# Kernel tuning notes

Measured on AMD Instinct MI355X. Metric: run time of the kernel, lower is better.

The kernel has to match this reference:

```python
import jax, jax.numpy as jnp
import numpy as np

D = 1024
H = 16
MODES = 16
EPS = 1e-5


def _layernorm(x, g, b):
    mu = jnp.mean(x, axis=-1, keepdims=True)
    var = jnp.var(x, axis=-1, keepdims=True)
    return (x - mu) * jax.lax.rsqrt(var + EPS) * g + b


def setup_inputs() -> dict:
    key = jax.random.key(0)
    ks = jax.random.split(key, 12)
    B, S = 32, 2048
    x_feat = jax.random.normal(ks[0], (B, S, D), dtype=jnp.float32)
    z_prev = jax.random.normal(ks[1], (B, D), dtype=jnp.float32)
    # MultiheadAttention params (torch packs q,k,v in in_proj)
    in_proj_w = jax.random.normal(ks[2], (3 * D, D), dtype=jnp.float32) * (1.0 / np.sqrt(D))
    in_proj_b = jnp.zeros((3 * D,), dtype=jnp.float32)
    out_proj_w = jax.random.normal(ks[3], (D, D), dtype=jnp.float32) * (1.0 / np.sqrt(D))
    out_proj_b = jnp.zeros((D,), dtype=jnp.float32)
    ln1_g = jnp.ones((D,), jnp.float32); ln1_b = jnp.zeros((D,), jnp.float32)
    ln2_g = jnp.ones((D,), jnp.float32); ln2_b = jnp.zeros((D,), jnp.float32)
    scale_real = jax.random.normal(ks[4], (MODES, D), dtype=jnp.float32) * 0.02
    scale_imag = jax.random.normal(ks[5], (MODES, D), dtype=jnp.float32) * 0.02
    # spectral_norm(Linear): effective weight = W / sigma_max(W); bake it in
    Wp = np.asarray(jax.random.normal(ks[6], (D, D), dtype=jnp.float32)) * (1.0 / np.sqrt(D))
    sigma = np.linalg.svd(Wp, compute_uv=False)[0]
    proj_w = jnp.asarray(Wp / sigma, dtype=jnp.float32)
    proj_b = jnp.zeros((D,), jnp.float32)
    bn_g = jnp.ones((D,), jnp.float32); bn_b = jnp.zeros((D,), jnp.float32)
    gate = jnp.asarray(0.5, jnp.float32)
    scale_attn = jnp.ones((1,), jnp.float32)
    scale_denoise = jnp.ones((1,), jnp.float32)
    return dict(x_feat=x_feat, z_prev=z_prev, in_proj_w=in_proj_w, in_proj_b=in_proj_b,
                out_proj_w=out_proj_w, out_proj_b=out_proj_b, ln1_g=ln1_g, ln1_b=ln1_b,
                ln2_g=ln2_g, ln2_b=ln2_b, scale_real=scale_real, scale_imag=scale_imag,
                proj_w=proj_w, proj_b=proj_b, bn_g=bn_g, bn_b=bn_b, gate=gate,
                scale_attn=scale_attn, scale_denoise=scale_denoise)


def reference(x_feat, z_prev, in_proj_w, in_proj_b, out_proj_w, out_proj_b,
              ln1_g, ln1_b, ln2_g, ln2_b, scale_real, scale_imag,
              proj_w, proj_b, bn_g, bn_b, gate, scale_attn, scale_denoise):
    B, S, _ = x_feat.shape
    hd = D // H
    Wq, Wk, Wv = in_proj_w[:D], in_proj_w[D:2 * D], in_proj_w[2 * D:]
    bq, bk, bv = in_proj_b[:D], in_proj_b[D:2 * D], in_proj_b[2 * D:]
    # single-query cross attention: q from z_prev [B,D], k/v from x_feat [B,S,D]
    q = (z_prev @ Wq.T + bq).reshape(B, H, hd)
    k = (x_feat @ Wk.T + bk).reshape(B, S, H, hd)
    v = (x_feat @ Wv.T + bv).reshape(B, S, H, hd)
    scores = jnp.einsum('bhd,bshd->bhs', q, k) / np.sqrt(hd)
    attn = jax.nn.softmax(scores, axis=-1)
    ctx = jnp.einsum('bhs,bshd->bhd', attn, v).reshape(B, D)
    attn_out = ctx @ out_proj_w.T + out_proj_b
    z1 = _layernorm(z_prev + scale_attn * attn_out, ln1_g, ln1_b)  # [B,D]
    # fft_denoise: keep first MODES freqs, each scaled by mean of its complex filter row
    filt = jnp.mean(scale_real + 1j * scale_imag, axis=1)  # [MODES] complex
    fvec = jnp.zeros((D,), dtype=jnp.complex64).at[:MODES].set(filt.astype(jnp.complex64))
    z_freq = jnp.fft.fft(z1, axis=1) * fvec[None, :]
    z_spatial = jnp.fft.ifft(z_freq, axis=1).real.astype(z1.dtype)
    denoised = z_spatial @ proj_w.T + proj_b
    z2 = _layernorm(z1 + scale_denoise * denoised, ln2_g, ln2_b)
    g = jax.nn.sigmoid(gate)
    z3 = g * z2 + (1.0 - g) * z_prev
    # BatchNorm1d (training-mode batch stats, biased variance)
    mu = jnp.mean(z3, axis=0, keepdims=True)
    var = jnp.var(z3, axis=0, keepdims=True)
    out = (z3 - mu) * jax.lax.rsqrt(var + EPS) * bn_g + bn_b
    return out
```

## Files before the change

### kernel.cpp

```cpp
#include <hip/hip_runtime.h>

#define B_ 32
#define S_ 2048
#define D_ 1024
#define H_ 16
#define HD_ 64
#define MODES_ 16
#define EPS_ 1e-5f

#define NSPLIT_ 16
#define RPB_ 128
#define RPI_ 32
#define NIT_ (RPB_ / RPI_)

#define OFF_CK      32
#define OFF_Q       1024
#define OFF_QKBF    33792
#define OFF_ML      295936
#define ML_L_OFF    8192
#define OFF_PART_F  312320
#define OFF_CTX     4506624
#define OFF_R1      4539392
#define OFF_Z1      4572160
#define OFF_ZSP     4604928
#define OFF_R2      4637696
#define OFF_Z3      4670464

typedef __attribute__((ext_vector_type(8))) short short8v;
typedef __attribute__((ext_vector_type(4))) float f32x4;

static __device__ inline unsigned short f2bf(float f) {
    union { float f; unsigned u; } v; v.f = f;
    unsigned r = v.u + 0x7FFFu + ((v.u >> 16) & 1u);
    return (unsigned short)(r >> 16);
}
static __device__ inline float bf2f(unsigned s) {
    union { unsigned u; float f; } v; v.u = s << 16;
    return v.f;
}

__global__ void k_q(const float* __restrict__ zprev, const float* __restrict__ ipw,
                    const float* __restrict__ ipb, float* __restrict__ q_out,
                    float* __restrict__ ck_out) {
    int b = blockIdx.x >> 2, nc = blockIdx.x & 3;
    __shared__ float zr[D_];
    int t = threadIdx.x;
    for (int i = t; i < D_; i += 256) zr[i] = zprev[(size_t)b * D_ + i];
    __syncthreads();
    int n = nc * 256 + t;
    const float4* wr = (const float4*)(ipw + (size_t)n * D_);
    float acc = 0.f;
    for (int k = 0; k < D_ / 4; ++k) {
        float4 wv = wr[k];
        float4 zv = *(const float4*)&zr[4 * k];
        acc = fmaf(zv.x, wv.x, acc); acc = fmaf(zv.y, wv.y, acc);
        acc = fmaf(zv.z, wv.z, acc); acc = fmaf(zv.w, wv.w, acc);
    }
    float qv = acc + ipb[n];
    q_out[(size_t)b * D_ + n] = qv;
    float cv = qv * ipb[D_ + n];
#pragma unroll
    for (int o = 32; o > 0; o >>= 1) cv += __shfl_xor(cv, o);
    if ((t & 63) == 0) ck_out[b * H_ + (n >> 6)] = cv;
}

__global__ void k_qkc(const float* __restrict__ ipw, const float* __restrict__ q_in,
                      unsigned short* __restrict__ qk_out) {
    int bid = blockIdx.x;
    int bc = bid & 3, nc = (bid >> 2) & 3, h = bid >> 4;
    int t = threadIdx.x;
    __shared__ float4 tile4[HD_ * 64];
    __shared__ float qall[8 * HD_];
    const float4* wk4 = (const float4*)(ipw + (size_t)D_ * D_);
#pragma unroll
    for (int j = 0; j < 16; ++j) {
        int lin4 = j * 256 + t;
        int i = lin4 >> 6, n4 = lin4 & 63;
        tile4[lin4] = wk4[(size_t)(h * HD_ + i) * 256 + nc * 64 + n4];
    }
#pragma unroll
    for (int j = 0; j < 2; ++j) {
        int idx = j * 256 + t;
        int bb = idx >> 6, i = idx & 63;
        qall[idx] = q_in[(size_t)(bc * 8 + bb) * D_ + h * HD_ + i];
    }
    __syncthreads();
    const float* tile = (const float*)tile4;
#pragma unroll
    for (int bb = 0; bb < 8; ++bb) {
        float acc = 0.f;
#pragma unroll
        for (int i = 0; i < HD_; ++i) acc = fmaf(qall[bb * HD_ + i], tile[i * 256 + t], acc);
        int b = bc * 8 + bb;
        qk_out[(size_t)(b * H_ + h) * D_ + nc * 256 + t] = f2bf(acc);
    }
}

__global__ __launch_bounds__(256, 2) void k_attn(const float* __restrict__ xfeat,
        const unsigned short* __restrict__ qkbf, const float* __restrict__ ck,
        unsigned short* __restrict__ part, float* __restrict__ ml) {
    int bid = blockIdx.x;
    int c = bid & (NSPLIT_ - 1), b = bid >> 4;
    int t = threadIdx.x, w = t >> 6, l = t & 63;
    __shared__ unsigned char xbuf[RPI_ * 2048];
    __shared__ float Sred[4][RPI_][16];
    __shared__ unsigned short Pt[16][RPI_];
    __shared__ float mh[16], lh[16], fh[16], ckl[16];

    if (t < 16) { mh[t] = -1e30f; lh[t] = 0.f; ckl[t] = ck[b * H_ + t]; }

    f32x4 acc[16];
#pragma unroll
    for (int nt = 0; nt < 16; ++nt) acc[nt] = (f32x4){0.f, 0.f, 0.f, 0.f};

    int hr = l & 15, kg = l >> 4;
    const unsigned short* qkb = qkbf + ((size_t)(b * H_ + hr) << 10);

    for (int it = 0; it < NIT_; ++it) {
        __syncthreads();
        {
            const float4* src = (const float4*)(xfeat + ((size_t)b * S_ + c * RPB_ + it * RPI_) * D_);
#pragma unroll 4
            for (int j = 0; j < 32; ++j) {
                int idx = j * 256 + t;
                float4 v = src[idx];
                int row = idx >> 8, dq = idx & 255;
                unsigned off = (unsigned)(row * 2048 + dq * 8) ^ (unsigned)((row & 7) << 4);
                ushort4 u;
                u.x = f2bf(v.x); u.y = f2bf(v.y); u.z = f2bf(v.z); u.w = f2bf(v.w);
                *(ushort4*)(xbuf + off) = u;
            }
        }
        __syncthreads();
        {
            f32x4 s0 = {0.f, 0.f, 0.f, 0.f}, s1 = {0.f, 0.f, 0.f, 0.f};
#pragma unroll
            for (int ks = 0; ks < 8; ++ks) {
                int k = w * 256 + ks * 32 + kg * 8;
                short8v bq = *(const short8v*)(qkb + k);
                unsigned off0 = (unsigned)(hr * 2048 + k * 2) ^ (unsigned)((hr & 7) << 4);
                short8v a0 = *(const short8v*)(xbuf + off0);
                short8v a1 = *(const short8v*)(xbuf + (off0 ^ 32768u));
                s0 = __builtin_amdgcn_mfma_f32_16x16x32_bf16(a0, bq, s0, 0, 0, 0);
                s1 = __builtin_amdgcn_mfma_f32_16x16x32_bf16(a1, bq, s1, 0, 0, 0);
            }
            int rbase = kg * 4;
#pragma unroll
            for (int r = 0; r < 4; ++r) {
                Sred[w][rbase + r][hr] = s0[r];
                Sred[w][16 + rbase + r][hr] = s1[r];
            }
        }
        __syncthreads();
        {
            int h = t >> 4, i16 = t & 15;
            float sv0 = Sred[0][i16][h] + Sred[1][i16][h] + Sred[2][i16][h] + Sred[3][i16][h];
            float sv1 = Sred[0][i16 + 16][h] + Sred[1][i16 + 16][h] + Sred[2][i16 + 16][h] + Sred[3][i16 + 16][h];
            float s0 = (sv0 + ckl[h]) * 0.125f;
            float s1 = (sv1 + ckl[h]) * 0.125f;
            float mm = fmaxf(s0, s1);
#pragma unroll
            for (int o = 8; o > 0; o >>= 1) mm = fmaxf(mm, __shfl_xor(mm, o, 16));
            float mold = mh[h];
            float mnew = fmaxf(mold, mm);
            float p0 = __expf(s0 - mnew), p1 = __expf(s1 - mnew);
            Pt[h][i16] = f2bf(p0); Pt[h][i16 + 16] = f2bf(p1);
            float ps = p0 + p1;
#pragma unroll
            for (int o = 8; o > 0; o >>= 1) ps += __shfl_xor(ps, o, 16);
            if (i16 == 0) {
                float f = __expf(mold - mnew);
                fh[h] = f; lh[h] = lh[h] * f + ps; mh[h] = mnew;
            }
        }
        __syncthreads();
        {
            float f0 = fh[kg * 4 + 0], f1 = fh[kg * 4 + 1], f2 = fh[kg * 4 + 2], f3 = fh[kg * 4 + 3];
#pragma unroll
            for (int nt = 0; nt < 16; ++nt) {
                acc[nt][0] *= f0; acc[nt][1] *= f1; acc[nt][2] *= f2; acc[nt][3] *= f3;
            }
            short8v pa = *(const short8v*)(&Pt[hr][kg * 8]);
#pragma unroll
            for (int nt = 0; nt < 16; ++nt) {
                int d = w * 256 + nt * 16 + hr;
                unsigned short xb[8];
#pragma unroll
                for (int j = 0; j < 8; ++j) {
                    int s = kg * 8 + j;
                    unsigned off = (unsigned)(s * 2048 + d * 2) ^ (unsigned)((s & 7) << 4);
                    xb[j] = *(const unsigned short*)(xbuf + off);
                }
                short8v bx;
                bx[0] = (short)xb[0]; bx[1] = (short)xb[1]; bx[2] = (short)xb[2]; bx[3] = (short)xb[3];
                bx[4] = (short)xb[4]; bx[5] = (short)xb[5]; bx[6] = (short)xb[6]; bx[7] = (short)xb[7];
                acc[nt] = __builtin_amdgcn_mfma_f32_16x16x32_bf16(pa, bx, acc[nt], 0, 0, 0);
            }
        }
    }
    {
#pragma unroll
        for (int nt = 0; nt < 16; ++nt) {
            int d = w * 256 + nt * 16 + hr;
#pragma unroll
            for (int r = 0; r < 4; ++r) {
                int h = kg * 4 + r;
                part[(((size_t)(c * B_ + b) * H_ + h) << 10) + d] = f2bf(acc[nt][r]);
            }
        }
        if (t < 16) {
            ml[(size_t)(c * B_ + b) * H_ + t] = mh[t];
            ml[ML_L_OFF + (size_t)(c * B_ + b) * H_ + t] = lh[t];
        }
    }
}

__global__ void k_ctx2(const float* __restrict__ ipw, const float* __restrict__ ipb,
                       const unsigned short* __restrict__ part, const float* __restrict__ ml,
                       float* __restrict__ ctx) {
    int b = blockIdx.x >> 2, nc = blockIdx.x & 3;
    int t = threadIdx.x;
    __shared__ float mls[4][16], lls[4][16], coef[4][16];
    __shared__ float xr[4 * D_];
    if (t < 64) {
        int h4 = t >> 4, c = t & 15;
        mls[h4][c] = ml[(size_t)(c * B_ + b) * H_ + nc * 4 + h4];
        lls[h4][c] = ml[ML_L_OFF + (size_t)(c * B_ + b) * H_ + nc * 4 + h4];
    }
    __syncthreads();
    if (t < 4) {
        float M = -1e30f;
        for (int c = 0; c < 16; ++c) M = fmaxf(M, mls[t][c]);
        float L = 0.f;
        for (int c = 0; c < 16; ++c) L += lls[t][c] * __expf(mls[t][c] - M);
        float invL = 1.f / L;
        for (int c = 0; c < 16; ++c) coef[t][c] = __expf(mls[t][c] - M) * invL;
    }
    __syncthreads();
    for (int idx = t * 2; idx < 4 * D_; idx += 512) {
        int h4 = idx >> 10, d = idx & 1023;
        int h = nc * 4 + h4;
        float a0 = 0.f, a1 = 0.f;
        for (int c = 0; c < 16; ++c) {
            unsigned u = *(const unsigned*)&part[(((size_t)(c * B_ + b) * H_ + h) << 10) + d];
            float cf = coef[h4][c];
            a0 = fmaf(bf2f(u & 0xffffu), cf, a0);
            a1 = fmaf(bf2f(u >> 16), cf, a1);
        }
        xr[idx] = a0; xr[idx + 1] = a1;
    }
    __syncthreads();
    int n = nc * 256 + t;
    int hl = t >> 6;
    const float4* wr = (const float4*)(ipw + ((size_t)2 * D_ + n) * D_);
    const float4* xv4 = (const float4*)&xr[hl * D_];
    float acc = 0.f;
    for (int k = 0; k < D_ / 4; ++k) {
        float4 wv = wr[k], xv = xv4[k];
        acc = fmaf(wv.x, xv.x, acc); acc = fmaf(wv.y, xv.y, acc);
        acc = fmaf(wv.z, xv.z, acc); acc = fmaf(wv.w, xv.w, acc);
    }
    ctx[(size_t)b * D_ + n] = acc + ipb[2 * D_ + n];
}

__global__ void k_proj_res(const float* __restrict__ wmat, const float* __restrict__ bias,
                           const float* __restrict__ scale, const float* __restrict__ resid,
                           const float* __restrict__ invec, float* __restrict__ outvec) {
    int b = blockIdx.x >> 2, nc = blockIdx.x & 3;
    __shared__ float cx[D_];
    int t = threadIdx.x;
    for (int i = t; i < D_; i += 256) cx[i] = invec[(size_t)b * D_ + i];
    __syncthreads();
    int n = nc * 256 + t;
    const float4* wr = (const float4*)(wmat + (size_t)n * D_);
    float acc = 0.f;
    for (int k = 0; k < D_ / 4; ++k) {
        float4 wv = wr[k];
        float4 cv = *(const float4*)&cx[4 * k];
        acc = fmaf(wv.x, cv.x, acc); acc = fmaf(wv.y, cv.y, acc);
        acc = fmaf(wv.z, cv.z, acc); acc = fmaf(wv.w, cv.w, acc);
    }
    outvec[(size_t)b * D_ + n] = resid[(size_t)b * D_ + n] + scale[0] * (acc + bias[n]);
}

__global__ void k_ln(const float* __restrict__ inv, const float* __restrict__ g,
                     const float* __restrict__ bv, float* __restrict__ outv) {
    int b = blockIdx.x, t = threadIdx.x, w = t >> 6, l = t & 63;
    float4 v = ((const float4*)(inv + (size_t)b * D_))[t];
    float s = v.x + v.y + v.z + v.w;
    float s2 = v.x * v.x + v.y * v.y + v.z * v.z + v.w * v.w;
    __shared__ float sa[4], sb[4];
#pragma unroll
    for (int o = 32; o > 0; o >>= 1) { s += __shfl_xor(s, o); s2 += __shfl_xor(s2, o); }
    if (l == 0) { sa[w] = s; sb[w] = s2; }
    __syncthreads();
    s = sa[0] + sa[1] + sa[2] + sa[3];
    s2 = sb[0] + sb[1] + sb[2] + sb[3];
    float mu = s * (1.f / (float)D_);
    float var = s2 * (1.f / (float)D_) - mu * mu;
    float rs = rsqrtf(var + EPS_);
    float4 gg = ((const float4*)g)[t], bb = ((const float4*)bv)[t];
    float4 o4;
    o4.x = (v.x - mu) * rs * gg.x + bb.x;
    o4.y = (v.y - mu) * rs * gg.y + bb.y;
    o4.z = (v.z - mu) * rs * gg.z + bb.z;
    o4.w = (v.w - mu) * rs * gg.w + bb.w;
    ((float4*)(outv + (size_t)b * D_))[t] = o4;
}

__global__ void k_spec(const float* __restrict__ sreal, const float* __restrict__ simag,
                       float* __restrict__ ws) {
    int b = blockIdx.x, t = threadIdx.x;
    __shared__ float zr[D_];
    __shared__ float fre[MODES_], fim[MODES_];
    __shared__ float cre[MODES_], cim[MODES_];
    const float* z1 = ws + OFF_Z1 + (size_t)b * D_;
    for (int i = t; i < D_; i += 256) zr[i] = z1[i];
    int m = t >> 4, sub = t & 15;
    {
        float ar = 0.f, ai = 0.f;
        for (int k = sub; k < D_; k += 16) { ar += sreal[m * D_ + k]; ai += simag[m * D_ + k]; }
#pragma unroll
        for (int o = 8; o > 0; o >>= 1) { ar += __shfl_xor(ar, o, 16); ai += __shfl_xor(ai, o, 16); }
        if (sub == 0) { fre[m] = ar * (1.f / (float)D_); fim[m] = ai * (1.f / (float)D_); }
    }
    __syncthreads();
    const float step = 6.283185307179586f / (float)D_;
    float ar = 0.f, ai = 0.f;
    for (int n = sub; n < D_; n += 16) {
        int idx = (m * n) & (D_ - 1);
        float sn, cs;
        __sincosf(step * (float)idx, &sn, &cs);
        float z = zr[n];
        ar = fmaf(z, cs, ar); ai = fmaf(-z, sn, ai);
    }
#pragma unroll
    for (int o = 8; o > 0; o >>= 1) { ar += __shfl_xor(ar, o, 16); ai += __shfl_xor(ai, o, 16); }
    if (sub == 0) {
        cre[m] = (fre[m] * ar - fim[m] * ai) * (1.f / (float)D_);
        cim[m] = (fre[m] * ai + fim[m] * ar) * (1.f / (float)D_);
    }
    __syncthreads();
    for (int n = t; n < D_; n += 256) {
        float acc = 0.f;
#pragma unroll
        for (int mm = 0; mm < MODES_; ++mm) {
            int idx = (mm * n) & (D_ - 1);
            float sn, cs;
            __sincosf(step * (float)idx, &sn, &cs);
            acc += cre[mm] * cs - cim[mm] * sn;
        }
        ws[OFF_ZSP + (size_t)b * D_ + n] = acc;
    }
}

__global__ void k_ln2gate(const float* __restrict__ zprev, const float* __restrict__ g2,
                          const float* __restrict__ b2v, const float* __restrict__ gate,
                          float* __restrict__ ws) {
    int b = blockIdx.x, t = threadIdx.x, w = t >> 6, l = t & 63;
    float4 v = ((const float4*)(ws + OFF_R2 + (size_t)b * D_))[t];
    float s = v.x + v.y + v.z + v.w;
    float s2 = v.x * v.x + v.y * v.y + v.z * v.z + v.w * v.w;
    __shared__ float sa[4], sb[4];
#pragma unroll
    for (int o = 32; o > 0; o >>= 1) { s += __shfl_xor(s, o); s2 += __shfl_xor(s2, o); }
    if (l == 0) { sa[w] = s; sb[w] = s2; }
    __syncthreads();
    s = sa[0] + sa[1] + sa[2] + sa[3];
    s2 = sb[0] + sb[1] + sb[2] + sb[3];
    float mu = s * (1.f / (float)D_);
    float var = s2 * (1.f / (float)D_) - mu * mu;
    float rs = rsqrtf(var + EPS_);
    float4 gg = ((const float4*)g2)[t], bb = ((const float4*)b2v)[t];
    float gsig = 1.f / (1.f + __expf(-gate[0]));
    float4 zp = ((const float4*)(zprev + (size_t)b * D_))[t];
    float4 z3;
    z3.x = gsig * ((v.x - mu) * rs * gg.x + bb.x) + (1.f - gsig) * zp.x;
    z3.y = gsig * ((v.y - mu) * rs * gg.y + bb.y) + (1.f - gsig) * zp.y;
    z3.z = gsig * ((v.z - mu) * rs * gg.z + bb.z) + (1.f - gsig) * zp.z;
    z3.w = gsig * ((v.w - mu) * rs * gg.w + bb.w) + (1.f - gsig) * zp.w;
    ((float4*)(ws + OFF_Z3 + (size_t)b * D_))[t] = z3;
}

__global__ void k_bn(const float* __restrict__ bng, const float* __restrict__ bnb,
                     const float* __restrict__ z3, float* __restrict__ out) {
    int d = blockIdx.x * 256 + threadIdx.x;
    float vals[B_];
    float s = 0.f, s2 = 0.f;
#pragma unroll
    for (int b = 0; b < B_; ++b) {
        float v = z3[(size_t)b * D_ + d];
        vals[b] = v; s += v; s2 = fmaf(v, v, s2);
    }
    float mu = s * (1.f / (float)B_);
    float var = s2 * (1.f / (float)B_) - mu * mu;
    float rs = rsqrtf(var + EPS_);
    float gg = bng[d], bb = bnb[d];
#pragma unroll
    for (int b = 0; b < B_; ++b) out[(size_t)b * D_ + d] = (vals[b] - mu) * rs * gg + bb;
}

extern "C" void kernel_launch(void* const* d_in, const int* in_sizes, int n_in,
                              void* d_out, int out_size, void* d_ws, size_t ws_size,
                              hipStream_t stream) {
    const float* x_feat = (const float*)d_in[0];
    const float* z_prev = (const float*)d_in[1];
    const float* ipw    = (const float*)d_in[2];
    const float* ipb    = (const float*)d_in[3];
    const float* wout   = (const float*)d_in[4];
    const float* bout   = (const float*)d_in[5];
    const float* ln1g   = (const float*)d_in[6];
    const float* ln1b   = (const float*)d_in[7];
    const float* ln2g   = (const float*)d_in[8];
    const float* ln2b   = (const float*)d_in[9];
    const float* sreal  = (const float*)d_in[10];
    const float* simag  = (const float*)d_in[11];
    const float* pw     = (const float*)d_in[12];
    const float* pb     = (const float*)d_in[13];
    const float* bng    = (const float*)d_in[14];
    const float* bnb    = (const float*)d_in[15];
    const float* gate   = (const float*)d_in[16];
    const float* sattn  = (const float*)d_in[17];
    const float* sden   = (const float*)d_in[18];
    float* ws  = (float*)d_ws;
    float* out = (float*)d_out;
    unsigned short* qkbf  = (unsigned short*)(ws + OFF_QKBF);
    unsigned short* partp = (unsigned short*)(ws + OFF_PART_F);

    k_q<<<B_ * 4, 256, 0, stream>>>(z_prev, ipw, ipb, ws + OFF_Q, ws + OFF_CK);
    k_qkc<<<H_ * 16, 256, 0, stream>>>(ipw, ws + OFF_Q, qkbf);
    k_attn<<<B_ * NSPLIT_, 256, 0, stream>>>(x_feat, qkbf, ws + OFF_CK, partp, ws + OFF_ML);
    k_ctx2<<<B_ * 4, 256, 0, stream>>>(ipw, ipb, partp, ws + OFF_ML, ws + OFF_CTX);
    k_proj_res<<<B_ * 4, 256, 0, stream>>>(wout, bout, sattn, z_prev, ws + OFF_CTX, ws + OFF_R1);
    k_ln<<<B_, 256, 0, stream>>>(ws + OFF_R1, ln1g, ln1b, ws + OFF_Z1);
    k_spec<<<B_, 256, 0, stream>>>(sreal, simag, ws);
    k_proj_res<<<B_ * 4, 256, 0, stream>>>(pw, pb, sden, ws + OFF_Z1, ws + OFF_ZSP, ws + OFF_R2);
    k_ln2gate<<<B_, 256, 0, stream>>>(z_prev, ln2g, ln2b, gate, ws);
    k_bn<<<D_ / 256, 256, 0, stream>>>(bng, bnb, ws + OFF_Z3, out);
}
```

Before: 259.5 us.

## Fuse layernorm with spectral filter and add ILP, hoisted Q fragments, packed bf16 converts

```diff
diff --git a/kernel.cpp b/kernel.cpp
--- a/kernel.cpp
+++ b/kernel.cpp
@@ -1,4 +1,5 @@
 #include <hip/hip_runtime.h>
+#include <hip/hip_bf16.h>
 
 #define B_ 32
 #define S_ 2048
@@ -29,10 +30,13 @@
 typedef __attribute__((ext_vector_type(8))) short short8v;
 typedef __attribute__((ext_vector_type(4))) float f32x4;
 
-static __device__ inline unsigned short f2bf(float f) {
-    union { float f; unsigned u; } v; v.f = f;
-    unsigned r = v.u + 0x7FFFu + ((v.u >> 16) & 1u);
-    return (unsigned short)(r >> 16);
+static __device__ inline ushort2 f2bf2(float a, float b) {
+    __hip_bfloat162 h = __float22bfloat162_rn(make_float2(a, b));
+    union { __hip_bfloat162 h; ushort2 u; } v; v.h = h; return v.u;
+}
+static __device__ inline unsigned short f2bf(float a) {
+    __hip_bfloat16 h = __float2bfloat16(a);
+    union { __hip_bfloat16 h; unsigned short u; } v; v.h = h; return v.u;
 }
 static __device__ inline float bf2f(unsigned s) {
     union { unsigned u; float f; } v; v.u = s << 16;
@@ -49,14 +53,19 @@
     __syncthreads();
     int n = nc * 256 + t;
     const float4* wr = (const float4*)(ipw + (size_t)n * D_);
-    float acc = 0.f;
-    for (int k = 0; k < D_ / 4; ++k) {
-        float4 wv = wr[k];
-        float4 zv = *(const float4*)&zr[4 * k];
-        acc = fmaf(zv.x, wv.x, acc); acc = fmaf(zv.y, wv.y, acc);
-        acc = fmaf(zv.z, wv.z, acc); acc = fmaf(zv.w, wv.w, acc);
-    }
-    float qv = acc + ipb[n];
+    float a0 = 0.f, a1 = 0.f, a2 = 0.f, a3 = 0.f;
+    for (int k = 0; k < 256; k += 4) {
+        float4 w0 = wr[k], w1 = wr[k + 1], w2 = wr[k + 2], w3 = wr[k + 3];
+        float4 z0 = *(const float4*)&zr[4 * k];
+        float4 z1 = *(const float4*)&zr[4 * k + 4];
+        float4 z2 = *(const float4*)&zr[4 * k + 8];
+        float4 z3 = *(const float4*)&zr[4 * k + 12];
+        a0 = fmaf(z0.x, w0.x, a0); a0 = fmaf(z0.y, w0.y, a0); a0 = fmaf(z0.z, w0.z, a0); a0 = fmaf(z0.w, w0.w, a0);
+        a1 = fmaf(z1.x, w1.x, a1); a1 = fmaf(z1.y, w1.y, a1); a1 = fmaf(z1.z, w1.z, a1); a1 = fmaf(z1.w, w1.w, a1);
+        a2 = fmaf(z2.x, w2.x, a2); a2 = fmaf(z2.y, w2.y, a2); a2 = fmaf(z2.z, w2.z, a2); a2 = fmaf(z2.w, w2.w, a2);
+        a3 = fmaf(z3.x, w3.x, a3); a3 = fmaf(z3.y, w3.y, a3); a3 = fmaf(z3.z, w3.z, a3); a3 = fmaf(z3.w, w3.w, a3);
+    }
+    float qv = (a0 + a1) + (a2 + a3) + ipb[n];
     q_out[(size_t)b * D_ + n] = qv;
     float cv = qv * ipb[D_ + n];
 #pragma unroll
@@ -88,11 +97,14 @@
     const float* tile = (const float*)tile4;
 #pragma unroll
     for (int bb = 0; bb < 8; ++bb) {
-        float acc = 0.f;
-#pragma unroll
-        for (int i = 0; i < HD_; ++i) acc = fmaf(qall[bb * HD_ + i], tile[i * 256 + t], acc);
+        float a0 = 0.f, a1 = 0.f;
+#pragma unroll
+        for (int i = 0; i < HD_; i += 2) {
+            a0 = fmaf(qall[bb * HD_ + i], tile[i * 256 + t], a0);
+            a1 = fmaf(qall[bb * HD_ + i + 1], tile[(i + 1) * 256 + t], a1);
+        }
         int b = bc * 8 + bb;
-        qk_out[(size_t)(b * H_ + h) * D_ + nc * 256 + t] = f2bf(acc);
+        qk_out[(size_t)(b * H_ + h) * D_ + nc * 256 + t] = f2bf(a0 + a1);
     }
 }
 
@@ -103,7 +115,7 @@
     int c = bid & (NSPLIT_ - 1), b = bid >> 4;
     int t = threadIdx.x, w = t >> 6, l = t & 63;
     __shared__ unsigned char xbuf[RPI_ * 2048];
-    __shared__ float Sred[4][RPI_][16];
+    __shared__ float Sred[4][RPI_][17];
     __shared__ unsigned short Pt[16][RPI_];
     __shared__ float mh[16], lh[16], fh[16], ckl[16];
 
@@ -115,19 +127,23 @@
 
     int hr = l & 15, kg = l >> 4;
     const unsigned short* qkb = qkbf + ((size_t)(b * H_ + hr) << 10);
+    short8v qfrag[8];
+#pragma unroll
+    for (int ks = 0; ks < 8; ++ks)
+        qfrag[ks] = *(const short8v*)(qkb + w * 256 + ks * 32 + kg * 8);
 
     for (int it = 0; it < NIT_; ++it) {
         __syncthreads();
         {
             const float4* src = (const float4*)(xfeat + ((size_t)b * S_ + c * RPB_ + it * RPI_) * D_);
-#pragma unroll 4
+#pragma unroll 8
             for (int j = 0; j < 32; ++j) {
                 int idx = j * 256 + t;
                 float4 v = src[idx];
                 int row = idx >> 8, dq = idx & 255;
                 unsigned off = (unsigned)(row * 2048 + dq * 8) ^ (unsigned)((row & 7) << 4);
-                ushort4 u;
-                u.x = f2bf(v.x); u.y = f2bf(v.y); u.z = f2bf(v.z); u.w = f2bf(v.w);
+                ushort2 lo = f2bf2(v.x, v.y), hi = f2bf2(v.z, v.w);
+                ushort4 u; u.x = lo.x; u.y = lo.y; u.z = hi.x; u.w = hi.y;
                 *(ushort4*)(xbuf + off) = u;
             }
         }
@@ -137,12 +153,11 @@
 #pragma unroll
             for (int ks = 0; ks < 8; ++ks) {
                 int k = w * 256 + ks * 32 + kg * 8;
-                short8v bq = *(const short8v*)(qkb + k);
                 unsigned off0 = (unsigned)(hr * 2048 + k * 2) ^ (unsigned)((hr & 7) << 4);
                 short8v a0 = *(const short8v*)(xbuf + off0);
                 short8v a1 = *(const short8v*)(xbuf + (off0 ^ 32768u));
-                s0 = __builtin_amdgcn_mfma_f32_16x16x32_bf16(a0, bq, s0, 0, 0, 0);
-                s1 = __builtin_amdgcn_mfma_f32_16x16x32_bf16(a1, bq, s1, 0, 0, 0);
+                s0 = __builtin_amdgcn_mfma_f32_16x16x32_bf16(a0, qfrag[ks], s0, 0, 0, 0);
+                s1 = __builtin_amdgcn_mfma_f32_16x16x32_bf16(a1, qfrag[ks], s1, 0, 0, 0);
             }
             int rbase = kg * 4;
 #pragma unroll
@@ -184,16 +199,13 @@
 #pragma unroll
             for (int nt = 0; nt < 16; ++nt) {
                 int d = w * 256 + nt * 16 + hr;
-                unsigned short xb[8];
+                short8v bx;
 #pragma unroll
                 for (int j = 0; j < 8; ++j) {
                     int s = kg * 8 + j;
                     unsigned off = (unsigned)(s * 2048 + d * 2) ^ (unsigned)((s & 7) << 4);
-                    xb[j] = *(const unsigned short*)(xbuf + off);
+                    bx[j] = *(const short*)(xbuf + off);
                 }
-                short8v bx;
-                bx[0] = (short)xb[0]; bx[1] = (short)xb[1]; bx[2] = (short)xb[2]; bx[3] = (short)xb[3];
-                bx[4] = (short)xb[4]; bx[5] = (short)xb[5]; bx[6] = (short)xb[6]; bx[7] = (short)xb[7];
                 acc[nt] = __builtin_amdgcn_mfma_f32_16x16x32_bf16(pa, bx, acc[nt], 0, 0, 0);
             }
         }
@@ -254,13 +266,16 @@
     int hl = t >> 6;
     const float4* wr = (const float4*)(ipw + ((size_t)2 * D_ + n) * D_);
     const float4* xv4 = (const float4*)&xr[hl * D_];
-    float acc = 0.f;
-    for (int k = 0; k < D_ / 4; ++k) {
-        float4 wv = wr[k], xv = xv4[k];
-        acc = fmaf(wv.x, xv.x, acc); acc = fmaf(wv.y, xv.y, acc);
-        acc = fmaf(wv.z, xv.z, acc); acc = fmaf(wv.w, xv.w, acc);
-    }
-    ctx[(size_t)b * D_ + n] = acc + ipb[2 * D_ + n];
+    float a0 = 0.f, a1 = 0.f, a2 = 0.f, a3 = 0.f;
+    for (int k = 0; k < 256; k += 4) {
+        float4 w0 = wr[k], w1 = wr[k + 1], w2 = wr[k + 2], w3 = wr[k + 3];
+        float4 x0 = xv4[k], x1 = xv4[k + 1], x2 = xv4[k + 2], x3 = xv4[k + 3];
+        a0 = fmaf(w0.x, x0.x, a0); a0 = fmaf(w0.y, x0.y, a0); a0 = fmaf(w0.z, x0.z, a0); a0 = fmaf(w0.w, x0.w, a0);
+        a1 = fmaf(w1.x, x1.x, a1); a1 = fmaf(w1.y, x1.y, a1); a1 = fmaf(w1.z, x1.z, a1); a1 = fmaf(w1.w, x1.w, a1);
+        a2 = fmaf(w2.x, x2.x, a2); a2 = fmaf(w2.y, x2.y, a2); a2 = fmaf(w2.z, x2.z, a2); a2 = fmaf(w2.w, x2.w, a2);
+        a3 = fmaf(w3.x, x3.x, a3); a3 = fmaf(w3.y, x3.y, a3); a3 = fmaf(w3.z, x3.z, a3); a3 = fmaf(w3.w, x3.w, a3);
+    }
+    ctx[(size_t)b * D_ + n] = (a0 + a1) + (a2 + a3) + ipb[2 * D_ + n];
 }
 
 __global__ void k_proj_res(const float* __restrict__ wmat, const float* __restrict__ bias,
@@ -273,72 +288,76 @@
     __syncthreads();
     int n = nc * 256 + t;
     const float4* wr = (const float4*)(wmat + (size_t)n * D_);
-    float acc = 0.f;
-    for (int k = 0; k < D_ / 4; ++k) {
-        float4 wv = wr[k];
-        float4 cv = *(const float4*)&cx[4 * k];
-        acc = fmaf(wv.x, cv.x, acc); acc = fmaf(wv.y, cv.y, acc);
-        acc = fmaf(wv.z, cv.z, acc); acc = fmaf(wv.w, cv.w, acc);
-    }
+    float a0 = 0.f, a1 = 0.f, a2 = 0.f, a3 = 0.f;
+    for (int k = 0; k < 256; k += 4) {
+        float4 w0 = wr[k], w1 = wr[k + 1], w2 = wr[k + 2], w3 = wr[k + 3];
+        float4 c0 = *(const float4*)&cx[4 * k];
+        float4 c1 = *(const float4*)&cx[4 * k + 4];
+        float4 c2 = *(const float4*)&cx[4 * k + 8];
+        float4 c3 = *(const float4*)&cx[4 * k + 12];
+        a0 = fmaf(w0.x, c0.x, a0); a0 = fmaf(w0.y, c0.y, a0); a0 = fmaf(w0.z, c0.z, a0); a0 = fmaf(w0.w, c0.w, a0);
+        a1 = fmaf(w1.x, c1.x, a1); a1 = fmaf(w1.y, c1.y, a1); a1 = fmaf(w1.z, c1.z, a1); a1 = fmaf(w1.w, c1.w, a1);
+        a2 = fmaf(w2.x, c2.x, a2); a2 = fmaf(w2.y, c2.y, a2); a2 = fmaf(w2.z, c2.z, a2); a2 = fmaf(w2.w, c2.w, a2);
+        a3 = fmaf(w3.x, c3.x, a3); a3 = fmaf(w3.y, c3.y, a3); a3 = fmaf(w3.z, c3.z, a3); a3 = fmaf(w3.w, c3.w, a3);
+    }
+    float acc = (a0 + a1) + (a2 + a3);
     outvec[(size_t)b * D_ + n] = resid[(size_t)b * D_ + n] + scale[0] * (acc + bias[n]);
 }
 
-__global__ void k_ln(const float* __restrict__ inv, const float* __restrict__ g,
-                     const float* __restrict__ bv, float* __restrict__ outv) {
+__global__ void k_lnspec(const float* __restrict__ r1, const float* __restrict__ g1,
+                         const float* __restrict__ b1, const float* __restrict__ sreal,
+                         const float* __restrict__ simag, float* __restrict__ z1out,
+                         float* __restrict__ zspout) {
     int b = blockIdx.x, t = threadIdx.x, w = t >> 6, l = t & 63;
-    float4 v = ((const float4*)(inv + (size_t)b * D_))[t];
+    __shared__ float zr[D_];
+    __shared__ float fre[MODES_], fim[MODES_];
+    __shared__ float cre[MODES_], cim[MODES_];
+    __shared__ float sa[4], sb[4];
+    float4 v = ((const float4*)(r1 + (size_t)b * D_))[t];
     float s = v.x + v.y + v.z + v.w;
     float s2 = v.x * v.x + v.y * v.y + v.z * v.z + v.w * v.w;
-    __shared__ float sa[4], sb[4];
 #pragma unroll
     for (int o = 32; o > 0; o >>= 1) { s += __shfl_xor(s, o); s2 += __shfl_xor(s2, o); }
     if (l == 0) { sa[w] = s; sb[w] = s2; }
+    int m = t >> 4, sub = t & 15;
+    {
+        float ar = 0.f, ai = 0.f;
+        for (int k = sub; k < D_; k += 16) { ar += sreal[m * D_ + k]; ai += simag[m * D_ + k]; }
+#pragma unroll
+        for (int o = 8; o > 0; o >>= 1) { ar += __shfl_xor(ar, o, 16); ai += __shfl_xor(ai, o, 16); }
+        if (sub == 0) { fre[m] = ar * (1.f / (float)D_); fim[m] = ai * (1.f / (float)D_); }
+    }
     __syncthreads();
     s = sa[0] + sa[1] + sa[2] + sa[3];
     s2 = sb[0] + sb[1] + sb[2] + sb[3];
     float mu = s * (1.f / (float)D_);
     float var = s2 * (1.f / (float)D_) - mu * mu;
     float rs = rsqrtf(var + EPS_);
-    float4 gg = ((const float4*)g)[t], bb = ((const float4*)bv)[t];
-    float4 o4;
-    o4.x = (v.x - mu) * rs * gg.x + bb.x;
-    o4.y = (v.y - mu) * rs * gg.y + bb.y;
-    o4.z = (v.z - mu) * rs * gg.z + bb.z;
-    o4.w = (v.w - mu) * rs * gg.w + bb.w;
-    ((float4*)(outv + (size_t)b * D_))[t] = o4;
-}
-
-__global__ void k_spec(const float* __restrict__ sreal, const float* __restrict__ simag,
-                       float* __restrict__ ws) {
-    int b = blockIdx.x, t = threadIdx.x;
-    __shared__ float zr[D_];
-    __shared__ float fre[MODES_], fim[MODES_];
-    __shared__ float cre[MODES_], cim[MODES_];
-    const float* z1 = ws + OFF_Z1 + (size_t)b * D_;
-    for (int i = t; i < D_; i += 256) zr[i] = z1[i];
-    int m = t >> 4, sub = t & 15;
+    float4 gg = ((const float4*)g1)[t], bbv = ((const float4*)b1)[t];
+    float4 z4;
+    z4.x = (v.x - mu) * rs * gg.x + bbv.x;
+    z4.y = (v.y - mu) * rs * gg.y + bbv.y;
+    z4.z = (v.z - mu) * rs * gg.z + bbv.z;
+    z4.w = (v.w - mu) * rs * gg.w + bbv.w;
+    ((float4*)(z1out + (size_t)b * D_))[t] = z4;
+    *(float4*)&zr[4 * t] = z4;
+    __syncthreads();
+    const float step = 6.283185307179586f / (float)D_;
     {
         float ar = 0.f, ai = 0.f;
-        for (int k = sub; k < D_; k += 16) { ar += sreal[m * D_ + k]; ai += simag[m * D_ + k]; }
+        for (int n = sub; n < D_; n += 16) {
+            int idx = (m * n) & (D_ - 1);
+            float sn, cs;
+            __sincosf(step * (float)idx, &sn, &cs);
+            float z = zr[n];
+            ar = fmaf(z, cs, ar); ai = fmaf(-z, sn, ai);
+        }
 #pragma unroll
         for (int o = 8; o > 0; o >>= 1) { ar += __shfl_xor(ar, o, 16); ai += __shfl_xor(ai, o, 16); }
-        if (sub == 0) { fre[m] = ar * (1.f / (float)D_); fim[m] = ai * (1.f / (float)D_); }
-    }
-    __syncthreads();
-    const float step = 6.283185307179586f / (float)D_;
-    float ar = 0.f, ai = 0.f;
-    for (int n = sub; n < D_; n += 16) {
-        int idx = (m * n) & (D_ - 1);
-        float sn, cs;
-        __sincosf(step * (float)idx, &sn, &cs);
-        float z = zr[n];
-        ar = fmaf(z, cs, ar); ai = fmaf(-z, sn, ai);
-    }
-#pragma unroll
-    for (int o = 8; o > 0; o >>= 1) { ar += __shfl_xor(ar, o, 16); ai += __shfl_xor(ai, o, 16); }
-    if (sub == 0) {
-        cre[m] = (fre[m] * ar - fim[m] * ai) * (1.f / (float)D_);
-        cim[m] = (fre[m] * ai + fim[m] * ar) * (1.f / (float)D_);
+        if (sub == 0) {
+            cre[m] = (fre[m] * ar - fim[m] * ai) * (1.f / (float)D_);
+            cim[m] = (fre[m] * ai + fim[m] * ar) * (1.f / (float)D_);
+        }
     }
     __syncthreads();
     for (int n = t; n < D_; n += 256) {
@@ -350,7 +369,7 @@
             __sincosf(step * (float)idx, &sn, &cs);
             acc += cre[mm] * cs - cim[mm] * sn;
         }
-        ws[OFF_ZSP + (size_t)b * D_ + n] = acc;
+        zspout[(size_t)b * D_ + n] = acc;
     }
 }
 
@@ -432,8 +451,8 @@
     k_attn<<<B_ * NSPLIT_, 256, 0, stream>>>(x_feat, qkbf, ws + OFF_CK, partp, ws + OFF_ML);
     k_ctx2<<<B_ * 4, 256, 0, stream>>>(ipw, ipb, partp, ws + OFF_ML, ws + OFF_CTX);
     k_proj_res<<<B_ * 4, 256, 0, stream>>>(wout, bout, sattn, z_prev, ws + OFF_CTX, ws + OFF_R1);
-    k_ln<<<B_, 256, 0, stream>>>(ws + OFF_R1, ln1g, ln1b, ws + OFF_Z1);
-    k_spec<<<B_, 256, 0, stream>>>(sreal, simag, ws);
+    k_lnspec<<<B_, 256, 0, stream>>>(ws + OFF_R1, ln1g, ln1b, sreal, simag,
+                                     ws + OFF_Z1, ws + OFF_ZSP);
     k_proj_res<<<B_ * 4, 256, 0, stream>>>(pw, pb, sden, ws + OFF_Z1, ws + OFF_ZSP, ws + OFF_R2);
     k_ln2gate<<<B_, 256, 0, stream>>>(z_prev, ln2g, ln2b, gate, ws);
     k_bn<<<D_ / 256, 256, 0, stream>>>(bng, bnb, ws + OFF_Z3, out);
```

New measurement: 258.0 us. Within noise of the previous version (-0.6%).
